# Optimization experiments

Hardware: AMD Instinct MI355X
Metric: run time of the kernel (lower is better)

The kernel has to match this reference:

```python
import math
import jax, jax.numpy as jnp
import numpy as np

EPS = 1e-5
NUM_HEADER = 2


def pos_encoding(C, T, dtype):
    i = jnp.arange(C)
    exp = -((i - (i % 2)).astype(dtype) / C)
    freqs = jnp.power(jnp.asarray(10000.0, dtype), exp)[:, None]      # [C,1]
    phases = ((i % 2).astype(dtype) * (np.pi / 2))[:, None]           # [C,1]
    pos = jnp.arange(T, dtype=dtype)[None, :]                         # [1,T]
    return jnp.sin(pos * freqs + phases)                              # [C,T]


def layernorm2d(x, g, b):
    # LayerNorm over (C,T) jointly, per batch element (nn.LayerNorm([C, length]))
    mu = jnp.mean(x, axis=(1, 2), keepdims=True)
    var = jnp.mean((x - mu) ** 2, axis=(1, 2), keepdims=True)
    return (x - mu) * jax.lax.rsqrt(var + EPS) * g[None] + b[None]


def dsconv(x, dw_w, dw_b, pw_w, pw_b):
    # depthwise conv1d (groups=C, 'same' padding for odd k) + pointwise 1x1
    C = x.shape[1]
    k = dw_w.shape[-1]
    y = jax.lax.conv_general_dilated(
        x, dw_w[:, None, :], (1,), [(k // 2, k // 2)],
        dimension_numbers=('NCH', 'OIH', 'NCH'), feature_group_count=C)
    y = y + dw_b[None, :, None]
    y = jnp.einsum('bct,oc->bot', y, pw_w) + pw_b[None, :, None]
    return y


def attention(x, mask, Wq, Wk, Wv, Wo):
    # Faithful to source bug: all heads use Wqs[1]/Wks[1]/Wvs[1] -> identical heads.
    xt = jnp.transpose(x, (0, 2, 1))          # [B,T,C]
    C = xt.shape[-1]
    dk = C / NUM_HEADER
    q = xt @ Wq                               # [B,T,dk]
    k_ = xt @ Wk
    v = xt @ Wv
    s = jnp.einsum('bqd,bkd->bqk', q, k_) * (1.0 / math.sqrt(dk))
    hmask = mask[:, None, :]                  # mask over keys
    s = s * hmask + (1 - hmask) * (-1e30)
    a = jax.nn.softmax(s, axis=2) * mask[:, :, None]
    head = a @ v                              # [B,T,dk]
    heads = jnp.tile(head, (1, 1, NUM_HEADER))  # concat of identical heads
    out = heads @ Wo                          # [B,T,C]
    return jnp.transpose(out, (0, 2, 1))      # [B,C,T]


def setup_inputs() -> dict:
    key = jax.random.key(0)
    B, C, T = 16, 128, 1024
    NCONV, K = 4, 7
    dk = C // NUM_HEADER
    ks = jax.random.split(key, 12)
    inp = {
        'x': jax.random.normal(ks[0], (B, C, T), jnp.float32),
        'mask': jnp.ones((B, T), jnp.float32),
        'dw_w': jax.random.normal(ks[1], (NCONV, C, K), jnp.float32) * math.sqrt(2.0 / K),
        'dw_b': jnp.zeros((NCONV, C), jnp.float32),
        'pw_w': jax.random.normal(ks[2], (NCONV, C, C), jnp.float32) * math.sqrt(2.0 / C),
        'pw_b': jnp.zeros((NCONV, C), jnp.float32),
        'norm0_g': jnp.ones((C, T), jnp.float32),
        'norm0_b': jnp.zeros((C, T), jnp.float32),
        'norms_g': jnp.ones((NCONV, C, T), jnp.float32),
        'norms_b': jnp.zeros((NCONV, C, T), jnp.float32),
        'norme_g': jnp.ones((C, T), jnp.float32),
        'norme_b': jnp.zeros((C, T), jnp.float32),
        'Wq': jax.random.normal(ks[3], (C, dk), jnp.float32) * math.sqrt(2.0 / (C + dk)),
        'Wk': jax.random.normal(ks[4], (C, dk), jnp.float32) * math.sqrt(2.0 / (C + dk)),
        'Wv': jax.random.normal(ks[5], (C, dk), jnp.float32) * math.sqrt(2.0 / (C + dk)),
        'Wo': jax.random.normal(ks[6], (C, C), jnp.float32) * math.sqrt(2.0 / C),
        'fc_w': jax.random.normal(ks[7], (C, C), jnp.float32) * (0.1 * math.sqrt(6.0 / (2 * C))),
        'fc_b': jnp.zeros((C,), jnp.float32),
    }
    return inp


def reference(x, mask, dw_w, dw_b, pw_w, pw_b, norm0_g, norm0_b,
              norms_g, norms_b, norme_g, norme_b,
              Wq, Wk, Wv, Wo, fc_w, fc_b):
    B, C, T = x.shape
    nconv = dw_w.shape[0]
    # dropout is identity in eval mode (reference is deterministic)
    out = x + pos_encoding(C, T, x.dtype)[None]
    res = layernorm2d(out, norm0_g, norm0_b)
    for i in range(nconv):
        out = dsconv(out, dw_w[i], dw_b[i], pw_w[i], pw_b[i])
        out = jax.nn.relu(out)
        out = out + res
        res = out
        out = layernorm2d(out, norms_g[i], norms_b[i])
    out = attention(out, mask, Wq, Wk, Wv, Wo)
    out = out + res
    res = out
    out = layernorm2d(out, norme_g, norme_b)
    out = jnp.einsum('bct,oc->bot', out, fc_w) + fc_b[None, :, None]
    out = jax.nn.relu(out)
    out = out + res
    return out
```

## Files before the change

### kernel.cpp

```cpp
#include <hip/hip_runtime.h>
#include <math.h>

#define BB 16
#define CC 128
#define TT 1024
#define KK 7
#define DK 64
#define NSPLIT 4

typedef float f32x4 __attribute__((ext_vector_type(4)));
typedef short s16x8 __attribute__((ext_vector_type(8)));

__device__ inline short f2bf(float f) {
  union { float f; unsigned u; } v; v.f = f;
  unsigned r = (v.u + 0x7FFFu + ((v.u >> 16) & 1u)) >> 16;
  return (short)r;
}
__device__ inline float bf2f(short s) {
  union { unsigned u; float f; } v;
  v.u = ((unsigned)(unsigned short)s) << 16;
  return v.f;
}

__device__ inline void block_partial_256(float s, float ss, float* dst) {
#pragma unroll
  for (int off = 32; off; off >>= 1) { s += __shfl_xor(s, off); ss += __shfl_xor(ss, off); }
  __shared__ float red[8];
  int w = threadIdx.x >> 6;
  if ((threadIdx.x & 63) == 0) { red[2 * w] = s; red[2 * w + 1] = ss; }
  __syncthreads();
  if (threadIdx.x == 0) {
    for (int i = 1; i < 4; ++i) { s += red[2 * i]; ss += red[2 * i + 1]; }
    dst[0] = s; dst[1] = ss;
  }
}

__device__ inline void ln_stats_from_parts(const float* part_batch, int n, float* sh) {
  if (threadIdx.x < 64) {
    float s = 0.f, ss = 0.f;
    for (int i = threadIdx.x; i < n; i += 64) { s += part_batch[2 * i]; ss += part_batch[2 * i + 1]; }
#pragma unroll
    for (int off = 32; off; off >>= 1) { s += __shfl_xor(s, off); ss += __shfl_xor(ss, off); }
    if (threadIdx.x == 0) {
      const float invN = 1.f / (float)(CC * TT);
      float mu = s * invN;
      sh[0] = mu;
      sh[1] = rsqrtf(ss * invN - mu * mu + 1e-5f);
    }
  }
  __syncthreads();
}

__global__ __launch_bounds__(256) void k_prep(const float* __restrict__ pww,
                                              const float* __restrict__ Wq,
                                              const float* __restrict__ Wk,
                                              const float* __restrict__ Wv,
                                              const float* __restrict__ Wo,
                                              const float* __restrict__ fcw,
                                              const float* __restrict__ n0g,
                                              const float* __restrict__ n0b,
                                              const float* __restrict__ nsg,
                                              const float* __restrict__ nsb,
                                              const float* __restrict__ neg_,
                                              const float* __restrict__ neb,
                                              short* __restrict__ pwwb,
                                              short* __restrict__ wqkvb,
                                              short* __restrict__ wo2b,
                                              short* __restrict__ fcwb,
                                              short* __restrict__ lnpb) {
  int i = blockIdx.x * 256 + threadIdx.x;
  if (i < 65536) { pwwb[i] = f2bf(pww[i]); return; }
  i -= 65536;
  if (i < 24576) {
    int m = i >> 7, c = i & 127;
    int sel = m >> 6, d = m & 63;
    const float* srcp = sel == 0 ? Wq : (sel == 1 ? Wk : Wv);
    wqkvb[i] = f2bf(srcp[c * DK + d]);
    return;
  }
  i -= 24576;
  if (i < 8192) {
    int o = i >> 6, d = i & 63;
    wo2b[i] = f2bf(Wo[d * CC + o] + Wo[(d + 64) * CC + o]);
    return;
  }
  i -= 8192;
  if (i < 16384) { fcwb[i] = f2bf(fcw[i]); return; }
  i -= 16384;
  if (i >= 1572864) return;
  const int CT = CC * TT;
  float v;
  if (i < CT) v = n0g[i];
  else if (i < 2 * CT) v = n0b[i - CT];
  else if (i < 6 * CT) v = nsg[i - 2 * CT];
  else if (i < 10 * CT) v = nsb[i - 6 * CT];
  else if (i < 11 * CT) v = neg_[i - 10 * CT];
  else v = neb[i - 11 * CT];
  lnpb[i] = f2bf(v);
}

__global__ __launch_bounds__(256) void k_addpos(const float* __restrict__ x,
                                                short* __restrict__ out,
                                                float* __restrict__ part) {
  int bc = blockIdx.x;
  int c = bc & (CC - 1);
  float ce = (float)(c & ~1);
  float freq = expf(-(ce / (float)CC) * 9.210340371976184f);
  float phase = (c & 1) ? 1.5707963267948966f : 0.0f;
  const float4* xr = (const float4*)(x + (size_t)bc * TT);
  short* orow = out + (size_t)bc * TT;
  int t = threadIdx.x * 4;
  float4 xv = xr[threadIdx.x];
  float v0 = xv.x + sinf((float)t * freq + phase);
  float v1 = xv.y + sinf((float)(t + 1) * freq + phase);
  float v2 = xv.z + sinf((float)(t + 2) * freq + phase);
  float v3 = xv.w + sinf((float)(t + 3) * freq + phase);
  float s = v0 + v1 + v2 + v3;
  float ss = v0 * v0 + v1 * v1 + v2 * v2 + v3 * v3;
  short4 o; o.x = f2bf(v0); o.y = f2bf(v1); o.z = f2bf(v2); o.w = f2bf(v3);
  *(short4*)(orow + t) = o;
  block_partial_256(s, ss, part + (size_t)bc * 2);
}

template <bool LN_IN, bool LN_RES>
__global__ __launch_bounds__(256) void k_dsconv(const short* __restrict__ in,
                                                const short* __restrict__ lng,
                                                const short* __restrict__ lnb,
                                                const float* __restrict__ part_in, int npart,
                                                const float* __restrict__ dww,
                                                const float* __restrict__ dwb,
                                                const short* __restrict__ pwwb,
                                                const float* __restrict__ pwb,
                                                short* __restrict__ out,
                                                float* __restrict__ part_out) {
  int tile = blockIdx.x & 31, b = blockIdx.x >> 5;
  int t0 = tile * 32;
  __shared__ float stats[2];
  __shared__ float xs[CC][39];
  __shared__ __align__(16) short Dt[32][136];
  ln_stats_from_parts(part_in + (size_t)b * npart * 2, npart, stats);
  float mu = stats[0], rs = stats[1];

  for (int i = threadIdx.x; i < CC * 38; i += 256) {
    int c = i / 38, j = i - c * 38;
    int t = t0 + j - 3;
    float v = 0.f;
    if (t >= 0 && t < TT) {
      v = bf2f(in[((size_t)b * CC + c) * TT + t]);
      if (LN_IN) v = (v - mu) * rs * bf2f(lng[c * TT + t]) + bf2f(lnb[c * TT + t]);
    }
    xs[c][j] = v;
  }
  __syncthreads();
  for (int i = threadIdx.x; i < 32 * CC; i += 256) {
    int t = i >> 7, c = i & 127;
    float a = dwb[c];
#pragma unroll
    for (int j = 0; j < KK; ++j) a += dww[c * KK + j] * xs[c][t + j];
    Dt[t][c] = f2bf(a);
  }
  __syncthreads();

  int w = threadIdx.x >> 6, lane = threadIdx.x & 63;
  int lo = lane & 15, hi = lane >> 4;
  f32x4 acc[2][2];
#pragma unroll
  for (int mt = 0; mt < 2; ++mt)
#pragma unroll
    for (int nt = 0; nt < 2; ++nt) { acc[mt][nt][0] = 0.f; acc[mt][nt][1] = 0.f; acc[mt][nt][2] = 0.f; acc[mt][nt][3] = 0.f; }
#pragma unroll
  for (int ks = 0; ks < 4; ++ks) {
    s16x8 b0 = *(const s16x8*)&Dt[lo][ks * 32 + hi * 8];
    s16x8 b1 = *(const s16x8*)&Dt[16 + lo][ks * 32 + hi * 8];
    s16x8 a0 = *(const s16x8*)&pwwb[(size_t)(w * 32 + lo) * CC + ks * 32 + hi * 8];
    s16x8 a1 = *(const s16x8*)&pwwb[(size_t)(w * 32 + 16 + lo) * CC + ks * 32 + hi * 8];
    acc[0][0] = __builtin_amdgcn_mfma_f32_16x16x32_bf16(a0, b0, acc[0][0], 0, 0, 0);
    acc[0][1] = __builtin_amdgcn_mfma_f32_16x16x32_bf16(a0, b1, acc[0][1], 0, 0, 0);
    acc[1][0] = __builtin_amdgcn_mfma_f32_16x16x32_bf16(a1, b0, acc[1][0], 0, 0, 0);
    acc[1][1] = __builtin_amdgcn_mfma_f32_16x16x32_bf16(a1, b1, acc[1][1], 0, 0, 0);
  }

  float s = 0.f, ss = 0.f;
#pragma unroll
  for (int mt = 0; mt < 2; ++mt)
#pragma unroll
    for (int nt = 0; nt < 2; ++nt)
#pragma unroll
      for (int r = 0; r < 4; ++r) {
        int row = w * 32 + mt * 16 + hi * 4 + r;
        int t = t0 + nt * 16 + lo;
        float v = acc[mt][nt][r] + pwb[row];
        v = v > 0.f ? v : 0.f;
        size_t idx = ((size_t)b * CC + row) * TT + t;
        float rv = bf2f(in[idx]);
        if (LN_RES) rv = (rv - mu) * rs * bf2f(lng[row * TT + t]) + bf2f(lnb[row * TT + t]);
        v += rv;
        out[idx] = f2bf(v);
        s += v; ss += v * v;
      }
  block_partial_256(s, ss, part_out + (size_t)blockIdx.x * 2);
}

__global__ __launch_bounds__(256) void k_qkv(const short* __restrict__ in,
                                             const short* __restrict__ lng,
                                             const short* __restrict__ lnb,
                                             const float* __restrict__ part_in,
                                             const short* __restrict__ wqkvb,
                                             short* __restrict__ q,
                                             short* __restrict__ k,
                                             short* __restrict__ vt) {
  int tile = blockIdx.x & 31, b = blockIdx.x >> 5;
  int t0 = tile * 32;
  __shared__ float stats[2];
  __shared__ __align__(16) short Dt[32][136];
  ln_stats_from_parts(part_in + (size_t)b * 64, 32, stats);
  float mu = stats[0], rs = stats[1];
  for (int i = threadIdx.x; i < CC * 16; i += 256) {
    int c = i >> 4, t2 = (i & 15) * 2;
    size_t base = ((size_t)b * CC + c) * TT + t0 + t2;
    unsigned u = *(const unsigned*)(in + base);
    unsigned g = *(const unsigned*)(lng + c * TT + t0 + t2);
    unsigned bb2 = *(const unsigned*)(lnb + c * TT + t0 + t2);
    float v0 = (bf2f((short)(u & 0xFFFF)) - mu) * rs * bf2f((short)(g & 0xFFFF)) + bf2f((short)(bb2 & 0xFFFF));
    float v1 = (bf2f((short)(u >> 16)) - mu) * rs * bf2f((short)(g >> 16)) + bf2f((short)(bb2 >> 16));
    Dt[t2][c] = f2bf(v0);
    Dt[t2 + 1][c] = f2bf(v1);
  }
  __syncthreads();

  int w = threadIdx.x >> 6, lane = threadIdx.x & 63;
  int lo = lane & 15, hi = lane >> 4;
  f32x4 acc[3][2];
#pragma unroll
  for (int mt = 0; mt < 3; ++mt)
#pragma unroll
    for (int nt = 0; nt < 2; ++nt) { acc[mt][nt][0] = 0.f; acc[mt][nt][1] = 0.f; acc[mt][nt][2] = 0.f; acc[mt][nt][3] = 0.f; }
#pragma unroll
  for (int ks = 0; ks < 4; ++ks) {
    s16x8 b0 = *(const s16x8*)&Dt[lo][ks * 32 + hi * 8];
    s16x8 b1 = *(const s16x8*)&Dt[16 + lo][ks * 32 + hi * 8];
#pragma unroll
    for (int mt = 0; mt < 3; ++mt) {
      s16x8 a = *(const s16x8*)&wqkvb[(size_t)(w * 48 + mt * 16 + lo) * CC + ks * 32 + hi * 8];
      acc[mt][0] = __builtin_amdgcn_mfma_f32_16x16x32_bf16(a, b0, acc[mt][0], 0, 0, 0);
      acc[mt][1] = __builtin_amdgcn_mfma_f32_16x16x32_bf16(a, b1, acc[mt][1], 0, 0, 0);
    }
  }
#pragma unroll
  for (int mt = 0; mt < 3; ++mt)
#pragma unroll
    for (int nt = 0; nt < 2; ++nt) {
      int m0 = w * 48 + mt * 16 + hi * 4;
      int t = t0 + nt * 16 + lo;
      short4 pk;
      pk.x = f2bf(acc[mt][nt][0]); pk.y = f2bf(acc[mt][nt][1]);
      pk.z = f2bf(acc[mt][nt][2]); pk.w = f2bf(acc[mt][nt][3]);
      if (m0 < 64) {
        *(short4*)(q + ((size_t)b * TT + t) * DK + m0) = pk;
      } else if (m0 < 128) {
        *(short4*)(k + ((size_t)b * TT + t) * DK + (m0 - 64)) = pk;
      } else {
        int d = m0 - 128;
        vt[((size_t)b * DK + d) * TT + t] = pk.x;
        vt[((size_t)b * DK + d + 1) * TT + t] = pk.y;
        vt[((size_t)b * DK + d + 2) * TT + t] = pk.z;
        vt[((size_t)b * DK + d + 3) * TT + t] = pk.w;
      }
    }
}

__global__ __launch_bounds__(128) void k_attn(const short* __restrict__ qb,
                                              const short* __restrict__ kbuf,
                                              const short* __restrict__ vtb,
                                              const float* __restrict__ mask,
                                              short* __restrict__ pacc,
                                              float* __restrict__ pml) {
  int sp = blockIdx.x & (NSPLIT - 1);
  int qt = (blockIdx.x >> 2) & 31;
  int b = blockIdx.x >> 7;
  int w = threadIdx.x >> 6, lane = threadIdx.x & 63;
  int lo = lane & 15, hi = lane >> 4;

  __shared__ __align__(16) short ks[64][72];
  __shared__ __align__(16) short vt[64][72];
  __shared__ __align__(16) short ps[2][16][68];
  __shared__ float ms[64];

  const short* qp = qb + ((size_t)b * TT + qt * 32 + w * 16 + lo) * DK + hi * 8;
  s16x8 aq0 = *(const s16x8*)qp;
  s16x8 aq1 = *(const s16x8*)(qp + 32);

  f32x4 acc[4];
  float m_i[4], l_i[4];
#pragma unroll
  for (int r = 0; r < 4; ++r) {
    m_i[r] = -3.0e38f; l_i[r] = 0.f;
#pragma unroll
    for (int nt = 0; nt < 4; ++nt) acc[nt][r] = 0.f;
  }
  const float scale = 0.125f;

  for (int kb2 = sp * (TT / 64 / NSPLIT); kb2 < (sp + 1) * (TT / 64 / NSPLIT); ++kb2) {
    __syncthreads();
    for (int i = threadIdx.x; i < 512; i += 128) {
      int r = i >> 3, ch = i & 7;
      *(s16x8*)&ks[r][ch * 8] =
          *(const s16x8*)(kbuf + ((size_t)b * TT + kb2 * 64 + r) * DK + ch * 8);
      *(s16x8*)&vt[r][ch * 8] =
          *(const s16x8*)(vtb + ((size_t)b * DK + r) * TT + kb2 * 64 + ch * 8);
    }
    if (threadIdx.x < 64) ms[threadIdx.x] = mask[(size_t)b * TT + kb2 * 64 + threadIdx.x];
    __syncthreads();

    f32x4 sc[4];
#pragma unroll
    for (int nt = 0; nt < 4; ++nt) {
      f32x4 z; z[0] = 0.f; z[1] = 0.f; z[2] = 0.f; z[3] = 0.f;
      s16x8 bk0 = *(const s16x8*)&ks[nt * 16 + lo][hi * 8];
      s16x8 bk1 = *(const s16x8*)&ks[nt * 16 + lo][32 + hi * 8];
      z = __builtin_amdgcn_mfma_f32_16x16x32_bf16(aq0, bk0, z, 0, 0, 0);
      z = __builtin_amdgcn_mfma_f32_16x16x32_bf16(aq1, bk1, z, 0, 0, 0);
      sc[nt] = z;
    }
#pragma unroll
    for (int nt = 0; nt < 4; ++nt) {
      float mv = ms[nt * 16 + lo];
      float addv = (1.f - mv) * -1e30f;
#pragma unroll
      for (int r = 0; r < 4; ++r) sc[nt][r] = sc[nt][r] * scale * mv + addv;
    }
    float alpha[4];
#pragma unroll
    for (int r = 0; r < 4; ++r) {
      float m0 = fmaxf(fmaxf(sc[0][r], sc[1][r]), fmaxf(sc[2][r], sc[3][r]));
#pragma unroll
      for (int off = 1; off < 16; off <<= 1) m0 = fmaxf(m0, __shfl_xor(m0, off));
      float mn = fmaxf(m_i[r], m0);
      alpha[r] = __expf(m_i[r] - mn);
      m_i[r] = mn;
    }
    float psum[4] = {0.f, 0.f, 0.f, 0.f};
#pragma unroll
    for (int nt = 0; nt < 4; ++nt)
#pragma unroll
      for (int r = 0; r < 4; ++r) {
        float p = __expf(sc[nt][r] - m_i[r]);
        psum[r] += p;
        ps[w][hi * 4 + r][nt * 16 + lo] = f2bf(p);
      }
#pragma unroll
    for (int r = 0; r < 4; ++r) {
      float sum = psum[r];
#pragma unroll
      for (int off = 1; off < 16; off <<= 1) sum += __shfl_xor(sum, off);
      l_i[r] = l_i[r] * alpha[r] + sum;
    }
#pragma unroll
    for (int nt = 0; nt < 4; ++nt)
#pragma unroll
      for (int r = 0; r < 4; ++r) acc[nt][r] *= alpha[r];

    s16x8 ap0 = *(const s16x8*)&ps[w][lo][hi * 8];
    s16x8 ap1 = *(const s16x8*)&ps[w][lo][32 + hi * 8];
#pragma unroll
    for (int nt = 0; nt < 4; ++nt) {
      s16x8 bv0 = *(const s16x8*)&vt[nt * 16 + lo][hi * 8];
      s16x8 bv1 = *(const s16x8*)&vt[nt * 16 + lo][32 + hi * 8];
      acc[nt] = __builtin_amdgcn_mfma_f32_16x16x32_bf16(ap0, bv0, acc[nt], 0, 0, 0);
      acc[nt] = __builtin_amdgcn_mfma_f32_16x16x32_bf16(ap1, bv1, acc[nt], 0, 0, 0);
    }
  }
#pragma unroll
  for (int r = 0; r < 4; ++r) {
    int row = qt * 32 + w * 16 + hi * 4 + r;
    size_t pb = (((size_t)b * TT + row) * NSPLIT + sp) * DK;
#pragma unroll
    for (int nt = 0; nt < 4; ++nt) pacc[pb + nt * 16 + lo] = f2bf(acc[nt][r]);
    if (lo == 0) {
      size_t mb = (((size_t)b * TT + row) * NSPLIT + sp) * 2;
      pml[mb] = m_i[r];
      pml[mb + 1] = l_i[r];
    }
  }
}

__global__ __launch_bounds__(256) void k_attnout(const short* __restrict__ pacc,
                                                 const float* __restrict__ pml,
                                                 const float* __restrict__ mask,
                                                 const short* __restrict__ wo2b,
                                                 const short* __restrict__ res,
                                                 short* __restrict__ out,
                                                 float* __restrict__ part_out) {
  int tile = blockIdx.x & 31, b = blockIdx.x >> 5;
  int t0 = tile * 32;
  __shared__ __align__(16) short Ht[32][72];
  {
    int row = threadIdx.x >> 3, d8 = threadIdx.x & 7;
    size_t rb = (size_t)b * TT + t0 + row;
    float m[NSPLIT], l[NSPLIT];
#pragma unroll
    for (int s = 0; s < NSPLIT; ++s) {
      m[s] = pml[(rb * NSPLIT + s) * 2];
      l[s] = pml[(rb * NSPLIT + s) * 2 + 1];
    }
    float M = fmaxf(fmaxf(m[0], m[1]), fmaxf(m[2], m[3]));
    float wgt[NSPLIT], L = 0.f;
#pragma unroll
    for (int s = 0; s < NSPLIT; ++s) { wgt[s] = __expf(m[s] - M); L += wgt[s] * l[s]; }
    float inv = mask[rb] / L;
    float o[8];
#pragma unroll
    for (int j = 0; j < 8; ++j) o[j] = 0.f;
#pragma unroll
    for (int s = 0; s < NSPLIT; ++s) {
      s16x8 pv = *(const s16x8*)(pacc + (rb * NSPLIT + s) * DK + d8 * 8);
#pragma unroll
      for (int j = 0; j < 8; ++j) o[j] += wgt[s] * bf2f(pv[j]);
    }
    s16x8 hv;
#pragma unroll
    for (int j = 0; j < 8; ++j) hv[j] = f2bf(o[j] * inv);
    *(s16x8*)&Ht[row][d8 * 8] = hv;
  }
  __syncthreads();

  int w = threadIdx.x >> 6, lane = threadIdx.x & 63;
  int lo = lane & 15, hi = lane >> 4;
  f32x4 acc[2][2];
#pragma unroll
  for (int mt = 0; mt < 2; ++mt)
#pragma unroll
    for (int nt = 0; nt < 2; ++nt) { acc[mt][nt][0] = 0.f; acc[mt][nt][1] = 0.f; acc[mt][nt][2] = 0.f; acc[mt][nt][3] = 0.f; }
#pragma unroll
  for (int ks = 0; ks < 2; ++ks) {
    s16x8 b0 = *(const s16x8*)&Ht[lo][ks * 32 + hi * 8];
    s16x8 b1 = *(const s16x8*)&Ht[16 + lo][ks * 32 + hi * 8];
    s16x8 a0 = *(const s16x8*)&wo2b[(size_t)(w * 32 + lo) * DK + ks * 32 + hi * 8];
    s16x8 a1 = *(const s16x8*)&wo2b[(size_t)(w * 32 + 16 + lo) * DK + ks * 32 + hi * 8];
    acc[0][0] = __builtin_amdgcn_mfma_f32_16x16x32_bf16(a0, b0, acc[0][0], 0, 0, 0);
    acc[0][1] = __builtin_amdgcn_mfma_f32_16x16x32_bf16(a0, b1, acc[0][1], 0, 0, 0);
    acc[1][0] = __builtin_amdgcn_mfma_f32_16x16x32_bf16(a1, b0, acc[1][0], 0, 0, 0);
    acc[1][1] = __builtin_amdgcn_mfma_f32_16x16x32_bf16(a1, b1, acc[1][1], 0, 0, 0);
  }
  float s = 0.f, ss = 0.f;
#pragma unroll
  for (int mt = 0; mt < 2; ++mt)
#pragma unroll
    for (int nt = 0; nt < 2; ++nt)
#pragma unroll
      for (int r = 0; r < 4; ++r) {
        int row = w * 32 + mt * 16 + hi * 4 + r;
        int t = t0 + nt * 16 + lo;
        size_t idx = ((size_t)b * CC + row) * TT + t;
        float v = acc[mt][nt][r] + bf2f(res[idx]);
        out[idx] = f2bf(v);
        s += v; ss += v * v;
      }
  block_partial_256(s, ss, part_out + (size_t)blockIdx.x * 2);
}

__global__ __launch_bounds__(256) void k_fc(const short* __restrict__ in,
                                            const short* __restrict__ lng,
                                            const short* __restrict__ lnb,
                                            const float* __restrict__ part_in,
                                            const short* __restrict__ fcwb,
                                            const float* __restrict__ fb,
                                            float* __restrict__ out) {
  int tile = blockIdx.x & 31, b = blockIdx.x >> 5;
  int t0 = tile * 32;
  __shared__ float stats[2];
  __shared__ __align__(16) short Dt[32][136];
  ln_stats_from_parts(part_in + (size_t)b * 64, 32, stats);
  float mu = stats[0], rs = stats[1];
  for (int i = threadIdx.x; i < CC * 16; i += 256) {
    int c = i >> 4, t2 = (i & 15) * 2;
    size_t base = ((size_t)b * CC + c) * TT + t0 + t2;
    unsigned u = *(const unsigned*)(in + base);
    unsigned g = *(const unsigned*)(lng + c * TT + t0 + t2);
    unsigned bb2 = *(const unsigned*)(lnb + c * TT + t0 + t2);
    float v0 = (bf2f((short)(u & 0xFFFF)) - mu) * rs * bf2f((short)(g & 0xFFFF)) + bf2f((short)(bb2 & 0xFFFF));
    float v1 = (bf2f((short)(u >> 16)) - mu) * rs * bf2f((short)(g >> 16)) + bf2f((short)(bb2 >> 16));
    Dt[t2][c] = f2bf(v0);
    Dt[t2 + 1][c] = f2bf(v1);
  }
  __syncthreads();

  int w = threadIdx.x >> 6, lane = threadIdx.x & 63;
  int lo = lane & 15, hi = lane >> 4;
  f32x4 acc[2][2];
#pragma unroll
  for (int mt = 0; mt < 2; ++mt)
#pragma unroll
    for (int nt = 0; nt < 2; ++nt) { acc[mt][nt][0] = 0.f; acc[mt][nt][1] = 0.f; acc[mt][nt][2] = 0.f; acc[mt][nt][3] = 0.f; }
#pragma unroll
  for (int ks = 0; ks < 4; ++ks) {
    s16x8 b0 = *(const s16x8*)&Dt[lo][ks * 32 + hi * 8];
    s16x8 b1 = *(const s16x8*)&Dt[16 + lo][ks * 32 + hi * 8];
    s16x8 a0 = *(const s16x8*)&fcwb[(size_t)(w * 32 + lo) * CC + ks * 32 + hi * 8];
    s16x8 a1 = *(const s16x8*)&fcwb[(size_t)(w * 32 + 16 + lo) * CC + ks * 32 + hi * 8];
    acc[0][0] = __builtin_amdgcn_mfma_f32_16x16x32_bf16(a0, b0, acc[0][0], 0, 0, 0);
    acc[0][1] = __builtin_amdgcn_mfma_f32_16x16x32_bf16(a0, b1, acc[0][1], 0, 0, 0);
    acc[1][0] = __builtin_amdgcn_mfma_f32_16x16x32_bf16(a1, b0, acc[1][0], 0, 0, 0);
    acc[1][1] = __builtin_amdgcn_mfma_f32_16x16x32_bf16(a1, b1, acc[1][1], 0, 0, 0);
  }
#pragma unroll
  for (int mt = 0; mt < 2; ++mt)
#pragma unroll
    for (int nt = 0; nt < 2; ++nt)
#pragma unroll
      for (int r = 0; r < 4; ++r) {
        int row = w * 32 + mt * 16 + hi * 4 + r;
        int t = t0 + nt * 16 + lo;
        size_t idx = ((size_t)b * CC + row) * TT + t;
        float v = acc[mt][nt][r] + fb[row];
        v = v > 0.f ? v : 0.f;
        out[idx] = v + bf2f(in[idx]);
      }
}

extern "C" void kernel_launch(void* const* d_in, const int* in_sizes, int n_in,
                              void* d_out, int out_size, void* d_ws, size_t ws_size,
                              hipStream_t stream) {
  const float* x    = (const float*)d_in[0];
  const float* mask = (const float*)d_in[1];
  const float* dww  = (const float*)d_in[2];
  const float* dwb  = (const float*)d_in[3];
  const float* pww  = (const float*)d_in[4];
  const float* pwb  = (const float*)d_in[5];
  const float* n0g  = (const float*)d_in[6];
  const float* n0b  = (const float*)d_in[7];
  const float* nsg  = (const float*)d_in[8];
  const float* nsb  = (const float*)d_in[9];
  const float* neg_ = (const float*)d_in[10];
  const float* neb  = (const float*)d_in[11];
  const float* Wq   = (const float*)d_in[12];
  const float* Wk   = (const float*)d_in[13];
  const float* Wv   = (const float*)d_in[14];
  const float* Wo   = (const float*)d_in[15];
  const float* fcw  = (const float*)d_in[16];
  const float* fcb  = (const float*)d_in[17];
  float* out = (float*)d_out;

  float* W = (float*)d_ws;
  const size_t NBCT = (size_t)BB * CC * TT;
  const size_t NBTD = (size_t)BB * TT * DK;
  const size_t CT = (size_t)CC * TT;
  float* PART0 = W;
  float* PARTS = W + 4096;
  float* PML   = W + 9216;
  short* OB    = (short*)(W + 140288);
  short* SB    = OB + NBCT;
  short* QB    = SB + NBCT;
  short* KB    = QB + NBTD;
  short* VT    = KB + NBTD;
  short* PACC  = VT + NBTD;
  short* PWWB  = PACC + NBTD * NSPLIT;
  short* WQKVB = PWWB + 65536;
  short* WO2B  = WQKVB + 24576;
  short* FCWB  = WO2B + 8192;
  short* LNPB  = FCWB + 16384;
  short* N0G = LNPB, *N0B = LNPB + CT;
  short* NSG0 = LNPB + 2 * CT;
  short* NSB0 = LNPB + 6 * CT;
  short* NEG = LNPB + 10 * CT, *NEB = LNPB + 11 * CT;

  k_prep<<<6592, 256, 0, stream>>>(pww, Wq, Wk, Wv, Wo, fcw,
                                   n0g, n0b, nsg, nsb, neg_, neb,
                                   PWWB, WQKVB, WO2B, FCWB, LNPB);
  k_addpos<<<BB * CC, 256, 0, stream>>>(x, OB, PART0);
  k_dsconv<false, true><<<BB * 32, 256, 0, stream>>>(
      OB, N0G, N0B, PART0, 128, dww, dwb, PWWB, pwb, SB, PARTS);
  k_dsconv<true, false><<<BB * 32, 256, 0, stream>>>(
      SB, NSG0, NSB0, PARTS, 32,
      dww + 1 * CC * KK, dwb + 1 * CC, PWWB + 1 * CC * CC, pwb + 1 * CC, OB, PARTS + 1024);
  k_dsconv<true, false><<<BB * 32, 256, 0, stream>>>(
      OB, NSG0 + CT, NSB0 + CT, PARTS + 1024, 32,
      dww + 2 * CC * KK, dwb + 2 * CC, PWWB + 2 * CC * CC, pwb + 2 * CC, SB, PARTS + 2048);
  k_dsconv<true, false><<<BB * 32, 256, 0, stream>>>(
      SB, NSG0 + 2 * CT, NSB0 + 2 * CT, PARTS + 2048, 32,
      dww + 3 * CC * KK, dwb + 3 * CC, PWWB + 3 * CC * CC, pwb + 3 * CC, OB, PARTS + 3072);
  k_qkv<<<BB * 32, 256, 0, stream>>>(OB, NSG0 + 3 * CT, NSB0 + 3 * CT, PARTS + 3072,
                                     WQKVB, QB, KB, VT);
  k_attn<<<BB * 32 * NSPLIT, 128, 0, stream>>>(QB, KB, VT, mask, PACC, PML);
  k_attnout<<<BB * 32, 256, 0, stream>>>(PACC, PML, mask, WO2B, OB, SB, PARTS + 4096);
  k_fc<<<BB * 32, 256, 0, stream>>>(SB, NEG, NEB, PARTS + 4096, FCWB, fcb, out);
}
```

Baseline: 229.1 us.

## Halve time tiles to 16, fuse prep with addpos, drop LDS staging in attention

Merges the weight-prep and positional-encoding kernels into one launch and halves the time tile in the conv, qkv, attnout and fc kernels from 32 to 16. This doubles the grid to 1024 blocks for better occupancy across compute units. The conv and LN input loads become 16-byte vector loads. The attention kernel reads K, V and mask straight from global memory instead of staging them in shared memory, which removes two barriers per key block. The trade-off is more redundant weight fetches per block, halo overhead in the conv, and possibly uncoalesced global reads in attention.

New measurement: 219.8 us. -4.1%, faster.

```diff
diff --git a/kernel.cpp b/kernel.cpp
--- a/kernel.cpp
+++ b/kernel.cpp
@@ -51,24 +51,48 @@
   __syncthreads();
 }
 
-__global__ __launch_bounds__(256) void k_prep(const float* __restrict__ pww,
-                                              const float* __restrict__ Wq,
-                                              const float* __restrict__ Wk,
-                                              const float* __restrict__ Wv,
-                                              const float* __restrict__ Wo,
-                                              const float* __restrict__ fcw,
-                                              const float* __restrict__ n0g,
-                                              const float* __restrict__ n0b,
-                                              const float* __restrict__ nsg,
-                                              const float* __restrict__ nsb,
-                                              const float* __restrict__ neg_,
-                                              const float* __restrict__ neb,
-                                              short* __restrict__ pwwb,
-                                              short* __restrict__ wqkvb,
-                                              short* __restrict__ wo2b,
-                                              short* __restrict__ fcwb,
-                                              short* __restrict__ lnpb) {
-  int i = blockIdx.x * 256 + threadIdx.x;
+__global__ __launch_bounds__(256) void k_prep_addpos(const float* __restrict__ x,
+                                                     const float* __restrict__ pww,
+                                                     const float* __restrict__ Wq,
+                                                     const float* __restrict__ Wk,
+                                                     const float* __restrict__ Wv,
+                                                     const float* __restrict__ Wo,
+                                                     const float* __restrict__ fcw,
+                                                     const float* __restrict__ n0g,
+                                                     const float* __restrict__ n0b,
+                                                     const float* __restrict__ nsg,
+                                                     const float* __restrict__ nsb,
+                                                     const float* __restrict__ neg_,
+                                                     const float* __restrict__ neb,
+                                                     short* __restrict__ out,
+                                                     float* __restrict__ part,
+                                                     short* __restrict__ pwwb,
+                                                     short* __restrict__ wqkvb,
+                                                     short* __restrict__ wo2b,
+                                                     short* __restrict__ fcwb,
+                                                     short* __restrict__ lnpb) {
+  if (blockIdx.x < BB * CC) {
+    int bc = blockIdx.x;
+    int c = bc & (CC - 1);
+    float ce = (float)(c & ~1);
+    float freq = expf(-(ce / (float)CC) * 9.210340371976184f);
+    float phase = (c & 1) ? 1.5707963267948966f : 0.0f;
+    const float4* xr = (const float4*)(x + (size_t)bc * TT);
+    short* orow = out + (size_t)bc * TT;
+    int t = threadIdx.x * 4;
+    float4 xv = xr[threadIdx.x];
+    float v0 = xv.x + sinf((float)t * freq + phase);
+    float v1 = xv.y + sinf((float)(t + 1) * freq + phase);
+    float v2 = xv.z + sinf((float)(t + 2) * freq + phase);
+    float v3 = xv.w + sinf((float)(t + 3) * freq + phase);
+    float s = v0 + v1 + v2 + v3;
+    float ss = v0 * v0 + v1 * v1 + v2 * v2 + v3 * v3;
+    short4 o; o.x = f2bf(v0); o.y = f2bf(v1); o.z = f2bf(v2); o.w = f2bf(v3);
+    *(short4*)(orow + t) = o;
+    block_partial_256(s, ss, part + (size_t)bc * 2);
+    return;
+  }
+  int i = (blockIdx.x - BB * CC) * 256 + threadIdx.x;
   if (i < 65536) { pwwb[i] = f2bf(pww[i]); return; }
   i -= 65536;
   if (i < 24576) {
@@ -99,29 +123,6 @@
   lnpb[i] = f2bf(v);
 }
 
-__global__ __launch_bounds__(256) void k_addpos(const float* __restrict__ x,
-                                                short* __restrict__ out,
-                                                float* __restrict__ part) {
-  int bc = blockIdx.x;
-  int c = bc & (CC - 1);
-  float ce = (float)(c & ~1);
-  float freq = expf(-(ce / (float)CC) * 9.210340371976184f);
-  float phase = (c & 1) ? 1.5707963267948966f : 0.0f;
-  const float4* xr = (const float4*)(x + (size_t)bc * TT);
-  short* orow = out + (size_t)bc * TT;
-  int t = threadIdx.x * 4;
-  float4 xv = xr[threadIdx.x];
-  float v0 = xv.x + sinf((float)t * freq + phase);
-  float v1 = xv.y + sinf((float)(t + 1) * freq + phase);
-  float v2 = xv.z + sinf((float)(t + 2) * freq + phase);
-  float v3 = xv.w + sinf((float)(t + 3) * freq + phase);
-  float s = v0 + v1 + v2 + v3;
-  float ss = v0 * v0 + v1 * v1 + v2 * v2 + v3 * v3;
-  short4 o; o.x = f2bf(v0); o.y = f2bf(v1); o.z = f2bf(v2); o.w = f2bf(v3);
-  *(short4*)(orow + t) = o;
-  block_partial_256(s, ss, part + (size_t)bc * 2);
-}
-
 template <bool LN_IN, bool LN_RES>
 __global__ __launch_bounds__(256) void k_dsconv(const short* __restrict__ in,
                                                 const short* __restrict__ lng,
@@ -133,140 +134,142 @@
                                                 const float* __restrict__ pwb,
                                                 short* __restrict__ out,
                                                 float* __restrict__ part_out) {
-  int tile = blockIdx.x & 31, b = blockIdx.x >> 5;
-  int t0 = tile * 32;
+  int tile = blockIdx.x & 63, b = blockIdx.x >> 6;
+  int t0 = tile * 16;
   __shared__ float stats[2];
-  __shared__ float xs[CC][39];
-  __shared__ __align__(16) short Dt[32][136];
+  __shared__ float xs[CC][33];
+  __shared__ __align__(16) short Dt[16][136];
   ln_stats_from_parts(part_in + (size_t)b * npart * 2, npart, stats);
   float mu = stats[0], rs = stats[1];
 
-  for (int i = threadIdx.x; i < CC * 38; i += 256) {
-    int c = i / 38, j = i - c * 38;
-    int t = t0 + j - 3;
-    float v = 0.f;
-    if (t >= 0 && t < TT) {
-      v = bf2f(in[((size_t)b * CC + c) * TT + t]);
-      if (LN_IN) v = (v - mu) * rs * bf2f(lng[c * TT + t]) + bf2f(lnb[c * TT + t]);
-    }
-    xs[c][j] = v;
-  }
-  __syncthreads();
-  for (int i = threadIdx.x; i < 32 * CC; i += 256) {
+  for (int ch = threadIdx.x; ch < 512; ch += 256) {
+    int c = ch >> 2, half = ch & 3;
+    int ts = t0 - 8 + half * 8;
+    float v[8];
+    if (ts >= 0 && ts < TT) {
+      size_t base = ((size_t)b * CC + c) * TT + ts;
+      s16x8 raw = *(const s16x8*)(in + base);
+      if (LN_IN) {
+        s16x8 g = *(const s16x8*)(lng + c * TT + ts);
+        s16x8 bb = *(const s16x8*)(lnb + c * TT + ts);
+#pragma unroll
+        for (int j = 0; j < 8; ++j)
+          v[j] = (bf2f(raw[j]) - mu) * rs * bf2f(g[j]) + bf2f(bb[j]);
+      } else {
+#pragma unroll
+        for (int j = 0; j < 8; ++j) v[j] = bf2f(raw[j]);
+      }
+    } else {
+#pragma unroll
+      for (int j = 0; j < 8; ++j) v[j] = 0.f;
+    }
+#pragma unroll
+    for (int j = 0; j < 8; ++j) xs[c][half * 8 + j] = v[j];
+  }
+  __syncthreads();
+  for (int i = threadIdx.x; i < 16 * CC; i += 256) {
     int t = i >> 7, c = i & 127;
     float a = dwb[c];
 #pragma unroll
-    for (int j = 0; j < KK; ++j) a += dww[c * KK + j] * xs[c][t + j];
+    for (int j = 0; j < KK; ++j) a += dww[c * KK + j] * xs[c][t + 5 + j];
     Dt[t][c] = f2bf(a);
   }
   __syncthreads();
 
   int w = threadIdx.x >> 6, lane = threadIdx.x & 63;
   int lo = lane & 15, hi = lane >> 4;
-  f32x4 acc[2][2];
-#pragma unroll
-  for (int mt = 0; mt < 2; ++mt)
-#pragma unroll
-    for (int nt = 0; nt < 2; ++nt) { acc[mt][nt][0] = 0.f; acc[mt][nt][1] = 0.f; acc[mt][nt][2] = 0.f; acc[mt][nt][3] = 0.f; }
+  f32x4 acc[2];
+#pragma unroll
+  for (int mt = 0; mt < 2; ++mt) { acc[mt][0] = 0.f; acc[mt][1] = 0.f; acc[mt][2] = 0.f; acc[mt][3] = 0.f; }
 #pragma unroll
   for (int ks = 0; ks < 4; ++ks) {
     s16x8 b0 = *(const s16x8*)&Dt[lo][ks * 32 + hi * 8];
-    s16x8 b1 = *(const s16x8*)&Dt[16 + lo][ks * 32 + hi * 8];
     s16x8 a0 = *(const s16x8*)&pwwb[(size_t)(w * 32 + lo) * CC + ks * 32 + hi * 8];
     s16x8 a1 = *(const s16x8*)&pwwb[(size_t)(w * 32 + 16 + lo) * CC + ks * 32 + hi * 8];
-    acc[0][0] = __builtin_amdgcn_mfma_f32_16x16x32_bf16(a0, b0, acc[0][0], 0, 0, 0);
-    acc[0][1] = __builtin_amdgcn_mfma_f32_16x16x32_bf16(a0, b1, acc[0][1], 0, 0, 0);
-    acc[1][0] = __builtin_amdgcn_mfma_f32_16x16x32_bf16(a1, b0, acc[1][0], 0, 0, 0);
-    acc[1][1] = __builtin_amdgcn_mfma_f32_16x16x32_bf16(a1, b1, acc[1][1], 0, 0, 0);
+    acc[0] = __builtin_amdgcn_mfma_f32_16x16x32_bf16(a0, b0, acc[0], 0, 0, 0);
+    acc[1] = __builtin_amdgcn_mfma_f32_16x16x32_bf16(a1, b0, acc[1], 0, 0, 0);
   }
 
   float s = 0.f, ss = 0.f;
 #pragma unroll
   for (int mt = 0; mt < 2; ++mt)
 #pragma unroll
-    for (int nt = 0; nt < 2; ++nt)
-#pragma unroll
-      for (int r = 0; r < 4; ++r) {
-        int row = w * 32 + mt * 16 + hi * 4 + r;
-        int t = t0 + nt * 16 + lo;
-        float v = acc[mt][nt][r] + pwb[row];
-        v = v > 0.f ? v : 0.f;
-        size_t idx = ((size_t)b * CC + row) * TT + t;
-        float rv = bf2f(in[idx]);
-        if (LN_RES) rv = (rv - mu) * rs * bf2f(lng[row * TT + t]) + bf2f(lnb[row * TT + t]);
-        v += rv;
-        out[idx] = f2bf(v);
-        s += v; ss += v * v;
-      }
+    for (int r = 0; r < 4; ++r) {
+      int row = w * 32 + mt * 16 + hi * 4 + r;
+      int t = t0 + lo;
+      float v = acc[mt][r] + pwb[row];
+      v = v > 0.f ? v : 0.f;
+      size_t idx = ((size_t)b * CC + row) * TT + t;
+      float rv = bf2f(in[idx]);
+      if (LN_RES) rv = (rv - mu) * rs * bf2f(lng[row * TT + t]) + bf2f(lnb[row * TT + t]);
+      v += rv;
+      out[idx] = f2bf(v);
+      s += v; ss += v * v;
+    }
   block_partial_256(s, ss, part_out + (size_t)blockIdx.x * 2);
 }
 
 __global__ __launch_bounds__(256) void k_qkv(const short* __restrict__ in,
                                              const short* __restrict__ lng,
                                              const short* __restrict__ lnb,
-                                             const float* __restrict__ part_in,
+                                             const float* __restrict__ part_in, int npart,
                                              const short* __restrict__ wqkvb,
                                              short* __restrict__ q,
                                              short* __restrict__ k,
                                              short* __restrict__ vt) {
-  int tile = blockIdx.x & 31, b = blockIdx.x >> 5;
-  int t0 = tile * 32;
+  int tile = blockIdx.x & 63, b = blockIdx.x >> 6;
+  int t0 = tile * 16;
   __shared__ float stats[2];
-  __shared__ __align__(16) short Dt[32][136];
-  ln_stats_from_parts(part_in + (size_t)b * 64, 32, stats);
+  __shared__ __align__(16) short Dt[16][136];
+  ln_stats_from_parts(part_in + (size_t)b * npart * 2, npart, stats);
   float mu = stats[0], rs = stats[1];
-  for (int i = threadIdx.x; i < CC * 16; i += 256) {
-    int c = i >> 4, t2 = (i & 15) * 2;
-    size_t base = ((size_t)b * CC + c) * TT + t0 + t2;
-    unsigned u = *(const unsigned*)(in + base);
-    unsigned g = *(const unsigned*)(lng + c * TT + t0 + t2);
-    unsigned bb2 = *(const unsigned*)(lnb + c * TT + t0 + t2);
-    float v0 = (bf2f((short)(u & 0xFFFF)) - mu) * rs * bf2f((short)(g & 0xFFFF)) + bf2f((short)(bb2 & 0xFFFF));
-    float v1 = (bf2f((short)(u >> 16)) - mu) * rs * bf2f((short)(g >> 16)) + bf2f((short)(bb2 >> 16));
-    Dt[t2][c] = f2bf(v0);
-    Dt[t2 + 1][c] = f2bf(v1);
+  {
+    int i = threadIdx.x;
+    int c = i >> 1, half = i & 1;
+    int ts = t0 + half * 8;
+    size_t base = ((size_t)b * CC + c) * TT + ts;
+    s16x8 raw = *(const s16x8*)(in + base);
+    s16x8 g = *(const s16x8*)(lng + c * TT + ts);
+    s16x8 bb = *(const s16x8*)(lnb + c * TT + ts);
+#pragma unroll
+    for (int j = 0; j < 8; ++j)
+      Dt[half * 8 + j][c] = f2bf((bf2f(raw[j]) - mu) * rs * bf2f(g[j]) + bf2f(bb[j]));
   }
   __syncthreads();
 
   int w = threadIdx.x >> 6, lane = threadIdx.x & 63;
   int lo = lane & 15, hi = lane >> 4;
-  f32x4 acc[3][2];
-#pragma unroll
-  for (int mt = 0; mt < 3; ++mt)
-#pragma unroll
-    for (int nt = 0; nt < 2; ++nt) { acc[mt][nt][0] = 0.f; acc[mt][nt][1] = 0.f; acc[mt][nt][2] = 0.f; acc[mt][nt][3] = 0.f; }
+  f32x4 acc[3];
+#pragma unroll
+  for (int mt = 0; mt < 3; ++mt) { acc[mt][0] = 0.f; acc[mt][1] = 0.f; acc[mt][2] = 0.f; acc[mt][3] = 0.f; }
 #pragma unroll
   for (int ks = 0; ks < 4; ++ks) {
     s16x8 b0 = *(const s16x8*)&Dt[lo][ks * 32 + hi * 8];
-    s16x8 b1 = *(const s16x8*)&Dt[16 + lo][ks * 32 + hi * 8];
 #pragma unroll
     for (int mt = 0; mt < 3; ++mt) {
       s16x8 a = *(const s16x8*)&wqkvb[(size_t)(w * 48 + mt * 16 + lo) * CC + ks * 32 + hi * 8];
-      acc[mt][0] = __builtin_amdgcn_mfma_f32_16x16x32_bf16(a, b0, acc[mt][0], 0, 0, 0);
-      acc[mt][1] = __builtin_amdgcn_mfma_f32_16x16x32_bf16(a, b1, acc[mt][1], 0, 0, 0);
-    }
-  }
-#pragma unroll
-  for (int mt = 0; mt < 3; ++mt)
-#pragma unroll
-    for (int nt = 0; nt < 2; ++nt) {
-      int m0 = w * 48 + mt * 16 + hi * 4;
-      int t = t0 + nt * 16 + lo;
-      short4 pk;
-      pk.x = f2bf(acc[mt][nt][0]); pk.y = f2bf(acc[mt][nt][1]);
-      pk.z = f2bf(acc[mt][nt][2]); pk.w = f2bf(acc[mt][nt][3]);
-      if (m0 < 64) {
-        *(short4*)(q + ((size_t)b * TT + t) * DK + m0) = pk;
-      } else if (m0 < 128) {
-        *(short4*)(k + ((size_t)b * TT + t) * DK + (m0 - 64)) = pk;
-      } else {
-        int d = m0 - 128;
-        vt[((size_t)b * DK + d) * TT + t] = pk.x;
-        vt[((size_t)b * DK + d + 1) * TT + t] = pk.y;
-        vt[((size_t)b * DK + d + 2) * TT + t] = pk.z;
-        vt[((size_t)b * DK + d + 3) * TT + t] = pk.w;
-      }
-    }
+      acc[mt] = __builtin_amdgcn_mfma_f32_16x16x32_bf16(a, b0, acc[mt], 0, 0, 0);
+    }
+  }
+#pragma unroll
+  for (int mt = 0; mt < 3; ++mt) {
+    int m0 = w * 48 + mt * 16 + hi * 4;
+    int t = t0 + lo;
+    short4 pk;
+    pk.x = f2bf(acc[mt][0]); pk.y = f2bf(acc[mt][1]);
+    pk.z = f2bf(acc[mt][2]); pk.w = f2bf(acc[mt][3]);
+    if (m0 < 64) {
+      *(short4*)(q + ((size_t)b * TT + t) * DK + m0) = pk;
+    } else if (m0 < 128) {
+      *(short4*)(k + ((size_t)b * TT + t) * DK + (m0 - 64)) = pk;
+    } else {
+      int d = m0 - 128;
+      vt[((size_t)b * DK + d) * TT + t] = pk.x;
+      vt[((size_t)b * DK + d + 1) * TT + t] = pk.y;
+      vt[((size_t)b * DK + d + 2) * TT + t] = pk.z;
+      vt[((size_t)b * DK + d + 3) * TT + t] = pk.w;
+    }
+  }
 }
 
 __global__ __launch_bounds__(128) void k_attn(const short* __restrict__ qb,
@@ -281,10 +284,7 @@
   int w = threadIdx.x >> 6, lane = threadIdx.x & 63;
   int lo = lane & 15, hi = lane >> 4;
 
-  __shared__ __align__(16) short ks[64][72];
-  __shared__ __align__(16) short vt[64][72];
-  __shared__ __align__(16) short ps[2][16][68];
-  __shared__ float ms[64];
+  __shared__ __align__(16) short ps[2][16][72];
 
   const short* qp = qb + ((size_t)b * TT + qt * 32 + w * 16 + lo) * DK + hi * 8;
   s16x8 aq0 = *(const s16x8*)qp;
@@ -301,33 +301,24 @@
   const float scale = 0.125f;
 
   for (int kb2 = sp * (TT / 64 / NSPLIT); kb2 < (sp + 1) * (TT / 64 / NSPLIT); ++kb2) {
-    __syncthreads();
-    for (int i = threadIdx.x; i < 512; i += 128) {
-      int r = i >> 3, ch = i & 7;
-      *(s16x8*)&ks[r][ch * 8] =
-          *(const s16x8*)(kbuf + ((size_t)b * TT + kb2 * 64 + r) * DK + ch * 8);
-      *(s16x8*)&vt[r][ch * 8] =
-          *(const s16x8*)(vtb + ((size_t)b * DK + r) * TT + kb2 * 64 + ch * 8);
-    }
-    if (threadIdx.x < 64) ms[threadIdx.x] = mask[(size_t)b * TT + kb2 * 64 + threadIdx.x];
-    __syncthreads();
-
     f32x4 sc[4];
+    float mv[4];
 #pragma unroll
     for (int nt = 0; nt < 4; ++nt) {
+      const short* kp = kbuf + ((size_t)b * TT + kb2 * 64 + nt * 16 + lo) * DK + hi * 8;
+      s16x8 bk0 = *(const s16x8*)kp;
+      s16x8 bk1 = *(const s16x8*)(kp + 32);
       f32x4 z; z[0] = 0.f; z[1] = 0.f; z[2] = 0.f; z[3] = 0.f;
-      s16x8 bk0 = *(const s16x8*)&ks[nt * 16 + lo][hi * 8];
-      s16x8 bk1 = *(const s16x8*)&ks[nt * 16 + lo][32 + hi * 8];
       z = __builtin_amdgcn_mfma_f32_16x16x32_bf16(aq0, bk0, z, 0, 0, 0);
       z = __builtin_amdgcn_mfma_f32_16x16x32_bf16(aq1, bk1, z, 0, 0, 0);
       sc[nt] = z;
+      mv[nt] = mask[(size_t)b * TT + kb2 * 64 + nt * 16 + lo];
     }
 #pragma unroll
     for (int nt = 0; nt < 4; ++nt) {
-      float mv = ms[nt * 16 + lo];
-      float addv = (1.f - mv) * -1e30f;
-#pragma unroll
-      for (int r = 0; r < 4; ++r) sc[nt][r] = sc[nt][r] * scale * mv + addv;
+      float addv = (1.f - mv[nt]) * -1e30f;
+#pragma unroll
+      for (int r = 0; r < 4; ++r) sc[nt][r] = sc[nt][r] * scale * mv[nt] + addv;
     }
     float alpha[4];
 #pragma unroll
@@ -364,8 +355,9 @@
     s16x8 ap1 = *(const s16x8*)&ps[w][lo][32 + hi * 8];
 #pragma unroll
     for (int nt = 0; nt < 4; ++nt) {
-      s16x8 bv0 = *(const s16x8*)&vt[nt * 16 + lo][hi * 8];
-      s16x8 bv1 = *(const s16x8*)&vt[nt * 16 + lo][32 + hi * 8];
+      const short* vp = vtb + ((size_t)b * DK + nt * 16 + lo) * TT + kb2 * 64 + hi * 8;
+      s16x8 bv0 = *(const s16x8*)vp;
+      s16x8 bv1 = *(const s16x8*)(vp + 32);
       acc[nt] = __builtin_amdgcn_mfma_f32_16x16x32_bf16(ap0, bv0, acc[nt], 0, 0, 0);
       acc[nt] = __builtin_amdgcn_mfma_f32_16x16x32_bf16(ap1, bv1, acc[nt], 0, 0, 0);
     }
@@ -391,10 +383,10 @@
                                                  const short* __restrict__ res,
                                                  short* __restrict__ out,
                                                  float* __restrict__ part_out) {
-  int tile = blockIdx.x & 31, b = blockIdx.x >> 5;
-  int t0 = tile * 32;
-  __shared__ __align__(16) short Ht[32][72];
-  {
+  int tile = blockIdx.x & 63, b = blockIdx.x >> 6;
+  int t0 = tile * 16;
+  __shared__ __align__(16) short Ht[16][72];
+  if (threadIdx.x < 128) {
     int row = threadIdx.x >> 3, d8 = threadIdx.x & 7;
     size_t rb = (size_t)b * TT + t0 + row;
     float m[NSPLIT], l[NSPLIT];
@@ -426,96 +418,83 @@
 
   int w = threadIdx.x >> 6, lane = threadIdx.x & 63;
   int lo = lane & 15, hi = lane >> 4;
-  f32x4 acc[2][2];
-#pragma unroll
-  for (int mt = 0; mt < 2; ++mt)
-#pragma unroll
-    for (int nt = 0; nt < 2; ++nt) { acc[mt][nt][0] = 0.f; acc[mt][nt][1] = 0.f; acc[mt][nt][2] = 0.f; acc[mt][nt][3] = 0.f; }
+  f32x4 acc[2];
+#pragma unroll
+  for (int mt = 0; mt < 2; ++mt) { acc[mt][0] = 0.f; acc[mt][1] = 0.f; acc[mt][2] = 0.f; acc[mt][3] = 0.f; }
 #pragma unroll
   for (int ks = 0; ks < 2; ++ks) {
     s16x8 b0 = *(const s16x8*)&Ht[lo][ks * 32 + hi * 8];
-    s16x8 b1 = *(const s16x8*)&Ht[16 + lo][ks * 32 + hi * 8];
     s16x8 a0 = *(const s16x8*)&wo2b[(size_t)(w * 32 + lo) * DK + ks * 32 + hi * 8];
     s16x8 a1 = *(const s16x8*)&wo2b[(size_t)(w * 32 + 16 + lo) * DK + ks * 32 + hi * 8];
-    acc[0][0] = __builtin_amdgcn_mfma_f32_16x16x32_bf16(a0, b0, acc[0][0], 0, 0, 0);
-    acc[0][1] = __builtin_amdgcn_mfma_f32_16x16x32_bf16(a0, b1, acc[0][1], 0, 0, 0);
-    acc[1][0] = __builtin_amdgcn_mfma_f32_16x16x32_bf16(a1, b0, acc[1][0], 0, 0, 0);
-    acc[1][1] = __builtin_amdgcn_mfma_f32_16x16x32_bf16(a1, b1, acc[1][1], 0, 0, 0);
+    acc[0] = __builtin_amdgcn_mfma_f32_16x16x32_bf16(a0, b0, acc[0], 0, 0, 0);
+    acc[1] = __builtin_amdgcn_mfma_f32_16x16x32_bf16(a1, b0, acc[1], 0, 0, 0);
   }
   float s = 0.f, ss = 0.f;
 #pragma unroll
   for (int mt = 0; mt < 2; ++mt)
 #pragma unroll
-    for (int nt = 0; nt < 2; ++nt)
-#pragma unroll
-      for (int r = 0; r < 4; ++r) {
-        int row = w * 32 + mt * 16 + hi * 4 + r;
-        int t = t0 + nt * 16 + lo;
-        size_t idx = ((size_t)b * CC + row) * TT + t;
-        float v = acc[mt][nt][r] + bf2f(res[idx]);
-        out[idx] = f2bf(v);
-        s += v; ss += v * v;
-      }
+    for (int r = 0; r < 4; ++r) {
+      int row = w * 32 + mt * 16 + hi * 4 + r;
+      int t = t0 + lo;
+      size_t idx = ((size_t)b * CC + row) * TT + t;
+      float v = acc[mt][r] + bf2f(res[idx]);
+      out[idx] = f2bf(v);
+      s += v; ss += v * v;
+    }
   block_partial_256(s, ss, part_out + (size_t)blockIdx.x * 2);
 }
 
 __global__ __launch_bounds__(256) void k_fc(const short* __restrict__ in,
                                             const short* __restrict__ lng,
                                             const short* __restrict__ lnb,
-                                            const float* __restrict__ part_in,
+                                            const float* __restrict__ part_in, int npart,
                                             const short* __restrict__ fcwb,
                                             const float* __restrict__ fb,
                                             float* __restrict__ out) {
-  int tile = blockIdx.x & 31, b = blockIdx.x >> 5;
-  int t0 = tile * 32;
+  int tile = blockIdx.x & 63, b = blockIdx.x >> 6;
+  int t0 = tile * 16;
   __shared__ float stats[2];
-  __shared__ __align__(16) short Dt[32][136];
-  ln_stats_from_parts(part_in + (size_t)b * 64, 32, stats);
+  __shared__ __align__(16) short Dt[16][136];
+  ln_stats_from_parts(part_in + (size_t)b * npart * 2, npart, stats);
   float mu = stats[0], rs = stats[1];
-  for (int i = threadIdx.x; i < CC * 16; i += 256) {
-    int c = i >> 4, t2 = (i & 15) * 2;
-    size_t base = ((size_t)b * CC + c) * TT + t0 + t2;
-    unsigned u = *(const unsigned*)(in + base);
-    unsigned g = *(const unsigned*)(lng + c * TT + t0 + t2);
-    unsigned bb2 = *(const unsigned*)(lnb + c * TT + t0 + t2);
-    float v0 = (bf2f((short)(u & 0xFFFF)) - mu) * rs * bf2f((short)(g & 0xFFFF)) + bf2f((short)(bb2 & 0xFFFF));
-    float v1 = (bf2f((short)(u >> 16)) - mu) * rs * bf2f((short)(g >> 16)) + bf2f((short)(bb2 >> 16));
-    Dt[t2][c] = f2bf(v0);
-    Dt[t2 + 1][c] = f2bf(v1);
+  {
+    int i = threadIdx.x;
+    int c = i >> 1, half = i & 1;
+    int ts = t0 + half * 8;
+    size_t base = ((size_t)b * CC + c) * TT + ts;
+    s16x8 raw = *(const s16x8*)(in + base);
+    s16x8 g = *(const s16x8*)(lng + c * TT + ts);
+    s16x8 bb = *(const s16x8*)(lnb + c * TT + ts);
+#pragma unroll
+    for (int j = 0; j < 8; ++j)
+      Dt[half * 8 + j][c] = f2bf((bf2f(raw[j]) - mu) * rs * bf2f(g[j]) + bf2f(bb[j]));
   }
   __syncthreads();
 
   int w = threadIdx.x >> 6, lane = threadIdx.x & 63;
   int lo = lane & 15, hi = lane >> 4;
-  f32x4 acc[2][2];
-#pragma unroll
-  for (int mt = 0; mt < 2; ++mt)
-#pragma unroll
-    for (int nt = 0; nt < 2; ++nt) { acc[mt][nt][0] = 0.f; acc[mt][nt][1] = 0.f; acc[mt][nt][2] = 0.f; acc[mt][nt][3] = 0.f; }
+  f32x4 acc[2];
+#pragma unroll
+  for (int mt = 0; mt < 2; ++mt) { acc[mt][0] = 0.f; acc[mt][1] = 0.f; acc[mt][2] = 0.f; acc[mt][3] = 0.f; }
 #pragma unroll
   for (int ks = 0; ks < 4; ++ks) {
     s16x8 b0 = *(const s16x8*)&Dt[lo][ks * 32 + hi * 8];
-    s16x8 b1 = *(const s16x8*)&Dt[16 + lo][ks * 32 + hi * 8];
     s16x8 a0 = *(const s16x8*)&fcwb[(size_t)(w * 32 + lo) * CC + ks * 32 + hi * 8];
     s16x8 a1 = *(const s16x8*)&fcwb[(size_t)(w * 32 + 16 + lo) * CC + ks * 32 + hi * 8];
-    acc[0][0] = __builtin_amdgcn_mfma_f32_16x16x32_bf16(a0, b0, acc[0][0], 0, 0, 0);
-    acc[0][1] = __builtin_amdgcn_mfma_f32_16x16x32_bf16(a0, b1, acc[0][1], 0, 0, 0);
-    acc[1][0] = __builtin_amdgcn_mfma_f32_16x16x32_bf16(a1, b0, acc[1][0], 0, 0, 0);
-    acc[1][1] = __builtin_amdgcn_mfma_f32_16x16x32_bf16(a1, b1, acc[1][1], 0, 0, 0);
+    acc[0] = __builtin_amdgcn_mfma_f32_16x16x32_bf16(a0, b0, acc[0], 0, 0, 0);
+    acc[1] = __builtin_amdgcn_mfma_f32_16x16x32_bf16(a1, b0, acc[1], 0, 0, 0);
   }
 #pragma unroll
   for (int mt = 0; mt < 2; ++mt)
 #pragma unroll
-    for (int nt = 0; nt < 2; ++nt)
-#pragma unroll
-      for (int r = 0; r < 4; ++r) {
-        int row = w * 32 + mt * 16 + hi * 4 + r;
-        int t = t0 + nt * 16 + lo;
-        size_t idx = ((size_t)b * CC + row) * TT + t;
-        float v = acc[mt][nt][r] + fb[row];
-        v = v > 0.f ? v : 0.f;
-        out[idx] = v + bf2f(in[idx]);
-      }
+    for (int r = 0; r < 4; ++r) {
+      int row = w * 32 + mt * 16 + hi * 4 + r;
+      int t = t0 + lo;
+      size_t idx = ((size_t)b * CC + row) * TT + t;
+      float v = acc[mt][r] + fb[row];
+      v = v > 0.f ? v : 0.f;
+      out[idx] = v + bf2f(in[idx]);
+    }
 }
 
 extern "C" void kernel_launch(void* const* d_in, const int* in_sizes, int n_in,
@@ -547,8 +526,8 @@
   const size_t CT = (size_t)CC * TT;
   float* PART0 = W;
   float* PARTS = W + 4096;
-  float* PML   = W + 9216;
-  short* OB    = (short*)(W + 140288);
+  float* PML   = W + 4096 + 5 * 2048;
+  short* OB    = (short*)(PML + 131072);
   short* SB    = OB + NBCT;
   short* QB    = SB + NBCT;
   short* KB    = QB + NBTD;
@@ -564,24 +543,23 @@
   short* NSB0 = LNPB + 6 * CT;
   short* NEG = LNPB + 10 * CT, *NEB = LNPB + 11 * CT;
 
-  k_prep<<<6592, 256, 0, stream>>>(pww, Wq, Wk, Wv, Wo, fcw,
-                                   n0g, n0b, nsg, nsb, neg_, neb,
-                                   PWWB, WQKVB, WO2B, FCWB, LNPB);
-  k_addpos<<<BB * CC, 256, 0, stream>>>(x, OB, PART0);
-  k_dsconv<false, true><<<BB * 32, 256, 0, stream>>>(
+  k_prep_addpos<<<BB * CC + 6592, 256, 0, stream>>>(
+      x, pww, Wq, Wk, Wv, Wo, fcw, n0g, n0b, nsg, nsb, neg_, neb,
+      OB, PART0, PWWB, WQKVB, WO2B, FCWB, LNPB);
+  k_dsconv<false, true><<<BB * 64, 256, 0, stream>>>(
       OB, N0G, N0B, PART0, 128, dww, dwb, PWWB, pwb, SB, PARTS);
-  k_dsconv<true, false><<<BB * 32, 256, 0, stream>>>(
-      SB, NSG0, NSB0, PARTS, 32,
-      dww + 1 * CC * KK, dwb + 1 * CC, PWWB + 1 * CC * CC, pwb + 1 * CC, OB, PARTS + 1024);
-  k_dsconv<true, false><<<BB * 32, 256, 0, stream>>>(
-      OB, NSG0 + CT, NSB0 + CT, PARTS + 1024, 32,
-      dww + 2 * CC * KK, dwb + 2 * CC, PWWB + 2 * CC * CC, pwb + 2 * CC, SB, PARTS + 2048);
-  k_dsconv<true, false><<<BB * 32, 256, 0, stream>>>(
-      SB, NSG0 + 2 * CT, NSB0 + 2 * CT, PARTS + 2048, 32,
-      dww + 3 * CC * KK, dwb + 3 * CC, PWWB + 3 * CC * CC, pwb + 3 * CC, OB, PARTS + 3072);
-  k_qkv<<<BB * 32, 256, 0, stream>>>(OB, NSG0 + 3 * CT, NSB0 + 3 * CT, PARTS + 3072,
+  k_dsconv<true, false><<<BB * 64, 256, 0, stream>>>(
+      SB, NSG0, NSB0, PARTS, 64,
+      dww + 1 * CC * KK, dwb + 1 * CC, PWWB + 1 * CC * CC, pwb + 1 * CC, OB, PARTS + 2048);
+  k_dsconv<true, false><<<BB * 64, 256, 0, stream>>>(
+      OB, NSG0 + CT, NSB0 + CT, PARTS + 2048, 64,
+      dww + 2 * CC * KK, dwb + 2 * CC, PWWB + 2 * CC * CC, pwb + 2 * CC, SB, PARTS + 4096);
+  k_dsconv<true, false><<<BB * 64, 256, 0, stream>>>(
+      SB, NSG0 + 2 * CT, NSB0 + 2 * CT, PARTS + 4096, 64,
+      dww + 3 * CC * KK, dwb + 3 * CC, PWWB + 3 * CC * CC, pwb + 3 * CC, OB, PARTS + 6144);
+  k_qkv<<<BB * 64, 256, 0, stream>>>(OB, NSG0 + 3 * CT, NSB0 + 3 * CT, PARTS + 6144, 64,
                                      WQKVB, QB, KB, VT);
   k_attn<<<BB * 32 * NSPLIT, 128, 0, stream>>>(QB, KB, VT, mask, PACC, PML);
-  k_attnout<<<BB * 32, 256, 0, stream>>>(PACC, PML, mask, WO2B, OB, SB, PARTS + 4096);
-  k_fc<<<BB * 32, 256, 0, stream>>>(SB, NEG, NEB, PARTS + 4096, FCWB, fcb, out);
-}
+  k_attnout<<<BB * 64, 256, 0, stream>>>(PACC, PML, mask, WO2B, OB, SB, PARTS + 8192);
+  k_fc<<<BB * 64, 256, 0, stream>>>(SB, NEG, NEB, PARTS + 8192, 64, FCWB, fcb, out);
+}
```
